# Performance work log

Hardware: AMD Instinct MI355X
Metric: run time of the kernel (lower is better)

Reference implementation:

```python
import jax, jax.numpy as jnp
import numpy as np

N, P, D_IN, K, D_H = 4, 20000, 1024, 8, 64


def setup_inputs() -> dict:
    key = jax.random.key(0)
    ks = jax.random.split(key, 10)
    inp = {
        "x": jax.random.normal(ks[0], (N, P, D_IN), dtype=jnp.float32),
        "centroids": jax.random.normal(ks[1], (K, D_IN), dtype=jnp.float32),
        # proj_pre: Linear(in_dim, 64) + ReLU  (W stored as [in, out])
        "W_pre": jax.random.normal(ks[2], (D_IN, D_H), dtype=jnp.float32) / np.sqrt(D_IN),
        "b_pre": jnp.zeros((D_H,), dtype=jnp.float32),
        # attention: Linear(64,32) -> Tanh -> Linear(32,1)
        "W_a1": jax.random.normal(ks[3], (D_H, 32), dtype=jnp.float32) / np.sqrt(D_H),
        "b_a1": jnp.zeros((32,), dtype=jnp.float32),
        "W_a2": jax.random.normal(ks[4], (32, 1), dtype=jnp.float32) / np.sqrt(32.0),
        "b_a2": jnp.zeros((1,), dtype=jnp.float32),
        # proj_out: Linear(64,32) + ReLU (+ Dropout, identity at eval)
        "W_out": jax.random.normal(ks[5], (D_H, 32), dtype=jnp.float32) / np.sqrt(D_H),
        "b_out": jnp.zeros((32,), dtype=jnp.float32),
    }
    return inp


def reference(x, centroids, W_pre, b_pre, W_a1, b_a1, W_a2, b_a2, W_out, b_out):
    # --- cdist-based hard cluster assignment ---------------------------------
    # ||x - c||: use the expanded form to avoid an [n,p,K,d] broadcast.
    x2 = jnp.sum(x * x, axis=-1)                       # [n, p]
    c2 = jnp.sum(centroids * centroids, axis=-1)       # [K]
    d2 = x2[..., None] + c2 - 2.0 * jnp.einsum('npd,kd->npk', x, centroids)
    dist = jnp.sqrt(jnp.maximum(d2, 0.0))              # [n, p, K]

    wc = jax.nn.softmax(1e7 / dist, axis=-1)           # softmax(1e7/dist)
    wc = (wc > 0.5).astype(x.dtype)                    # hard assignment
    # F.normalize(p=1, dim=1): divide by per-(n,K) patch count (eps=1e-12)
    wc = wc / jnp.maximum(jnp.sum(wc, axis=1, keepdims=True), 1e-12)
    mask = jnp.sum(wc, axis=1) == 0                    # [n, K] empty clusters

    # --- per-patch projection -------------------------------------------------
    xp = jax.nn.relu(x @ W_pre + b_pre)                # [n, p, 64]

    # --- cluster pooling + attention ------------------------------------------
    x_cls = jnp.einsum('npd,nph->nhd', xp, wc)         # [n, K, 64]
    A = (jnp.tanh(x_cls @ W_a1 + b_a1) @ W_a2 + b_a2)[..., 0]  # [n, K]
    A = jnp.where(mask, jnp.asarray(-100000.0, A.dtype), A)
    wa = jax.nn.softmax(A, axis=-1)                    # [n, K]
    pooled = jnp.einsum('nhd,nh->nd', x_cls, wa)       # [n, 64]

    enc_cls = jax.nn.relu(pooled @ W_out + b_out)      # [n, 32] (dropout = eval)
    enc_seq = xp.reshape(-1, xp.shape[-1])             # [(n*p), 64]
    return enc_cls, enc_seq, enc_seq
```

## Files before the change

kernel.cpp:

```cpp
#include <hip/hip_runtime.h>
#include <math.h>

#define N_  4
#define P_  20000
#define DIN 1024
#define K_  8
#define DH  64
#define BP  128
#define NT  5

typedef float  f32x4 __attribute__((ext_vector_type(4)));
typedef short  s16x8 __attribute__((ext_vector_type(8)));
typedef unsigned int u32x4 __attribute__((ext_vector_type(4)));
typedef unsigned short ushort_t;


union FragU { u32x4 u; s16x8 s; };

__global__ __launch_bounds__(512) void k_pre(const float* __restrict__ W_pre,
                                             const float* __restrict__ centroids,
                                             float* __restrict__ ws) {
  const int t = threadIdx.x;
  const int b = blockIdx.x;
  if (b < 80) {
    const int c = b;
    ushort_t* Bth = (ushort_t*)(ws + 4096);
    ushort_t* Btl = (ushort_t*)(ws + 45056);
    for (int d = t; d < DIN; d += 512) {
      float v = 0.f;
      if (c < 64)      v = W_pre[(size_t)d * DH + c];
      else if (c < 72) v = centroids[(size_t)(c - 64) * DIN + d];
      unsigned u = __float_as_uint(v);
      unsigned r = u + 0x7FFFu + ((u >> 16) & 1u);
      unsigned hb = r & 0xFFFF0000u;
      float lo = v - __uint_as_float(hb);
      unsigned ul = __float_as_uint(lo);
      unsigned rl = ul + 0x7FFFu + ((ul >> 16) & 1u);
      Bth[(size_t)c * DIN + d] = (ushort_t)(hb >> 16);
      Btl[(size_t)c * DIN + d] = (ushort_t)(rl >> 16);
    }
  } else {
    int* gcnt = (int*)(ws + 2048);
    for (int i = t; i < N_ * K_ * DH; i += 512) ws[i] = 0.f;
    if (t < N_ * K_) gcnt[t] = 0;
    const int w = t >> 6, lane = t & 63;
    float s = 0.f;
    for (int d = lane; d < DIN; d += 64) {
      float v = centroids[(size_t)w * DIN + d];
      s += v * v;
    }
    for (int off = 32; off > 0; off >>= 1) s += __shfl_down(s, off, 64);
    if (lane == 0) ws[2080 + w] = s;
  }
}

__device__ __forceinline__ void cvt_split(const f32x4 a0, const f32x4 a1,
                                          FragU& ah, FragU& al) {
  float f[8];
#pragma unroll
  for (int e = 0; e < 4; ++e) { f[e] = a0[e]; f[4 + e] = a1[e]; }
#pragma unroll
  for (int q = 0; q < 4; ++q) {
    const unsigned u0 = __float_as_uint(f[2 * q]);
    const unsigned u1 = __float_as_uint(f[2 * q + 1]);
    ah.u[q] = (u0 >> 16) | (u1 & 0xFFFF0000u);
    const float l0 = f[2 * q]     - __uint_as_float(u0 & 0xFFFF0000u);
    const float l1 = f[2 * q + 1] - __uint_as_float(u1 & 0xFFFF0000u);
    al.u[q] = (__float_as_uint(l0) >> 16) | (__float_as_uint(l1) & 0xFFFF0000u);
  }
}

__global__ __launch_bounds__(256, 3) void k_main(
    const float* __restrict__ x, const float* __restrict__ b_pre,
    float* __restrict__ out1, float* __restrict__ out2, float* __restrict__ ws) {
  __shared__ float xp[BP * 65];
  __shared__ float sc[BP * 9];
  __shared__ int   assign_s[BP];
  __shared__ int   cnt8[K_];

  const int t = threadIdx.x;
  const int w = t >> 6, l = t & 63;
  const int m = l & 15, q4 = l >> 4;
  const int n = blockIdx.y;
  const int p0 = blockIdx.x * BP;
  const int validP = (P_ - p0) < BP ? (P_ - p0) : BP;

  const ushort_t* Bth = (const ushort_t*)(ws + 4096);
  const ushort_t* Btl = (const ushort_t*)(ws + 45056);

  if (t < K_) cnt8[t] = 0;

  f32x4 acc[2][NT];
#pragma unroll
  for (int rg = 0; rg < 2; ++rg)
#pragma unroll
    for (int tl = 0; tl < NT; ++tl) acc[rg][tl] = (f32x4){0.f, 0.f, 0.f, 0.f};

  const int r0 = p0 + 32 * w + m;
  const int r1 = r0 + 16;
  const int g0 = r0 < P_ ? r0 : P_ - 1;
  const int g1 = r1 < P_ ? r1 : P_ - 1;
  const float* xbase = x + (size_t)n * P_ * DIN + q4 * 8;
  const float* ap0 = xbase + (size_t)g0 * DIN;
  const float* ap1 = xbase + (size_t)g1 * DIN;

  const ushort_t* bhp[NT];
  const ushort_t* blp[NT];
#pragma unroll
  for (int tl = 0; tl < NT; ++tl) {
    const size_t off = (size_t)(tl * 16 + m) * DIN + q4 * 8;
    bhp[tl] = Bth + off;
    blp[tl] = Btl + off;
  }

#pragma unroll 4
  for (int ks = 0; ks < 32; ++ks) {
    const int ko = ks * 32;
    const f32x4 a00 = *(const f32x4*)(ap0 + ko);
    const f32x4 a01 = *(const f32x4*)(ap0 + ko + 4);
    const f32x4 a10 = *(const f32x4*)(ap1 + ko);
    const f32x4 a11 = *(const f32x4*)(ap1 + ko + 4);
    FragU bh[NT], bl[NT];
#pragma unroll
    for (int tl = 0; tl < NT; ++tl) {
      bh[tl].u = *(const u32x4*)(bhp[tl] + ko);
      bl[tl].u = *(const u32x4*)(blp[tl] + ko);
    }
    FragU ah0, al0, ah1, al1;
    cvt_split(a00, a01, ah0, al0);
    cvt_split(a10, a11, ah1, al1);
#pragma unroll
    for (int tl = 0; tl < NT; ++tl) {
      acc[0][tl] = __builtin_amdgcn_mfma_f32_16x16x32_bf16(ah0.s, bh[tl].s, acc[0][tl], 0, 0, 0);
      acc[1][tl] = __builtin_amdgcn_mfma_f32_16x16x32_bf16(ah1.s, bh[tl].s, acc[1][tl], 0, 0, 0);
    }
#pragma unroll
    for (int tl = 0; tl < NT; ++tl) {
      acc[0][tl] = __builtin_amdgcn_mfma_f32_16x16x32_bf16(ah0.s, bl[tl].s, acc[0][tl], 0, 0, 0);
      acc[1][tl] = __builtin_amdgcn_mfma_f32_16x16x32_bf16(ah1.s, bl[tl].s, acc[1][tl], 0, 0, 0);
    }
#pragma unroll
    for (int tl = 0; tl < NT; ++tl) {
      acc[0][tl] = __builtin_amdgcn_mfma_f32_16x16x32_bf16(al0.s, bh[tl].s, acc[0][tl], 0, 0, 0);
      acc[1][tl] = __builtin_amdgcn_mfma_f32_16x16x32_bf16(al1.s, bh[tl].s, acc[1][tl], 0, 0, 0);
    }
  }

#pragma unroll
  for (int tl = 0; tl < 4; ++tl) {
    const int col = tl * 16 + m;
    const float bb = b_pre[col];
#pragma unroll
    for (int rg = 0; rg < 2; ++rg) {
#pragma unroll
      for (int r = 0; r < 4; ++r) {
        const int row = 32 * w + 16 * rg + (q4 << 2) + r;
        float v = acc[rg][tl][r] + bb;
        v = v > 0.f ? v : 0.f;
        xp[row * 65 + col] = v;
        if (row < validP) {
          const size_t o = (((size_t)(n * P_ + p0 + row)) << 6) + col;
          out1[o] = v;
          out2[o] = v;
        }
      }
    }
  }
  if (m < K_) {
    const float cc = ws[2080 + m];
#pragma unroll
    for (int rg = 0; rg < 2; ++rg)
#pragma unroll
      for (int r = 0; r < 4; ++r) {
        const int row = 32 * w + 16 * rg + (q4 << 2) + r;
        sc[row * 9 + m] = cc - 2.f * acc[rg][4][r];
      }
  }
  __syncthreads();

  if (t < BP) {
    int a = -1;
    if (t < validP) {
      float best = 3.4e38f; int bk = 0;
#pragma unroll
      for (int k = 0; k < K_; ++k) {
        const float v = sc[t * 9 + k];
        if (v < best) { best = v; bk = k; }
      }
      a = bk;
      atomicAdd(&cnt8[bk], 1);
    }
    assign_s[t] = a;
  }
  __syncthreads();

  for (int task = t; task < K_ * DH; task += 256) {
    const int k = task >> 6, j = task & 63;
    float s = 0.f;
    for (int p = 0; p < BP; ++p)
      s += (assign_s[p] == k) ? xp[p * 65 + j] : 0.f;
    if (s != 0.f) atomicAdd(&ws[(n * K_ + k) * DH + j], s);
  }
  if (t < K_ && cnt8[t] > 0) atomicAdd((int*)(ws + 2048) + n * K_ + t, cnt8[t]);
}

__global__ __launch_bounds__(256) void k_final(
    const float* __restrict__ W_a1, const float* __restrict__ b_a1,
    const float* __restrict__ W_a2, const float* __restrict__ b_a2,
    const float* __restrict__ W_out, const float* __restrict__ b_out,
    const float* __restrict__ ws, float* __restrict__ enc_cls) {
  __shared__ float xc[N_ * K_ * DH];
  __shared__ float zs[N_ * K_ * 32];
  __shared__ float wa[N_ * K_];
  __shared__ float As[N_ * K_];
  __shared__ int   cnts[N_ * K_];
  __shared__ float pooled[N_ * DH];
  const int t = threadIdx.x;
  const float* gsum = ws;
  const int* gcnt = (const int*)(ws + 2048);

  if (t < N_ * K_) cnts[t] = gcnt[t];
  __syncthreads();
  for (int i = t; i < N_ * K_ * DH; i += 256) {
    const int nk = i >> 6;
    const int c = cnts[nk];
    xc[i] = (c > 0) ? gsum[i] / (float)c : 0.f;
  }
  __syncthreads();
  for (int i = t; i < N_ * K_ * 32; i += 256) {
    const int nk = i >> 5, h = i & 31;
    float z = b_a1[h];
    for (int j = 0; j < DH; ++j) z += xc[nk * DH + j] * W_a1[j * 32 + h];
    zs[i] = tanhf(z) * W_a2[h];
  }
  __syncthreads();
  if (t < N_ * K_) {
    float a = b_a2[0];
    for (int h = 0; h < 32; ++h) a += zs[t * 32 + h];
    As[t] = (cnts[t] > 0) ? a : -100000.f;
  }
  __syncthreads();
  if (t < N_) {
    float mx = -3.4e38f;
    for (int k = 0; k < K_; ++k) mx = fmaxf(mx, As[t * K_ + k]);
    float ssum = 0.f;
    float e[K_];
    for (int k = 0; k < K_; ++k) { e[k] = expf(As[t * K_ + k] - mx); ssum += e[k]; }
    for (int k = 0; k < K_; ++k) wa[t * K_ + k] = e[k] / ssum;
  }
  __syncthreads();
  {
    const int n = t >> 6, j = t & 63;
    float s = 0.f;
    for (int k = 0; k < K_; ++k) s += xc[(n * K_ + k) * DH + j] * wa[n * K_ + k];
    pooled[t] = s;
  }
  __syncthreads();
  if (t < N_ * 32) {
    const int n = t >> 5, o = t & 31;
    float s = b_out[o];
    for (int j = 0; j < DH; ++j) s += pooled[n * DH + j] * W_out[j * 32 + o];
    enc_cls[n * 32 + o] = fmaxf(s, 0.f);
  }
}

extern "C" void kernel_launch(void* const* d_in, const int* in_sizes, int n_in,
                              void* d_out, int out_size, void* d_ws, size_t ws_size,
                              hipStream_t stream) {
  const float* x         = (const float*)d_in[0];
  const float* centroids = (const float*)d_in[1];
  const float* W_pre     = (const float*)d_in[2];
  const float* b_pre     = (const float*)d_in[3];
  const float* W_a1      = (const float*)d_in[4];
  const float* b_a1      = (const float*)d_in[5];
  const float* W_a2      = (const float*)d_in[6];
  const float* b_a2      = (const float*)d_in[7];
  const float* W_out     = (const float*)d_in[8];
  const float* b_out     = (const float*)d_in[9];

  float* out     = (float*)d_out;
  float* ws      = (float*)d_ws;
  float* enc_cls = out;
  float* out1    = out + N_ * 32;
  float* out2    = out + N_ * 32 + (size_t)N_ * P_ * DH;

  hipLaunchKernelGGL(k_pre, dim3(81), dim3(512), 0, stream, W_pre, centroids, ws);
  hipLaunchKernelGGL(k_main, dim3((P_ + BP - 1) / BP, N_), dim3(256), 0, stream,
                     x, b_pre, out1, out2, ws);
  hipLaunchKernelGGL(k_final, dim3(1), dim3(256), 0, stream,
                     W_a1, b_a1, W_a2, b_a2, W_out, b_out, ws, enc_cls);
}
```

Before: 554.3 us.

## Software-pipeline the MFMA k-loop with register double-buffered prefetch

Restructures the main GEMM k-loop into a two-stage software pipeline. The bf16 hi/lo weight fragments for the next step and the x fragments two steps ahead are loaded into alternating register buffers while the current step's MFMAs run. A sched_barrier separates the issued loads from the MFMA block. Launch bounds are relaxed from 3 to 2 waves per SIMD so the extra registers fit, trading occupancy for in-wave latency hiding.

```diff
diff --git a/kernel.cpp b/kernel.cpp
--- a/kernel.cpp
+++ b/kernel.cpp
@@ -70,7 +70,49 @@
   }
 }
 
-__global__ __launch_bounds__(256, 3) void k_main(
+template<bool PFB, bool PFX>
+__device__ __forceinline__ void kstep(
+    int kob, int kox,
+    FragU* bhC, FragU* blC, FragU* bhN, FragU* blN,
+    f32x4& X0, f32x4& X1, f32x4& X2, f32x4& X3,
+    const float* __restrict__ ap0, const float* __restrict__ ap1,
+    const ushort_t* const* bhp, const ushort_t* const* blp,
+    f32x4 acc[2][NT]) {
+  if (PFB) {
+#pragma unroll
+    for (int tl = 0; tl < NT; ++tl) {
+      bhN[tl].u = *(const u32x4*)(bhp[tl] + kob);
+      blN[tl].u = *(const u32x4*)(blp[tl] + kob);
+    }
+  }
+  FragU ah0, al0, ah1, al1;
+  cvt_split(X0, X1, ah0, al0);
+  cvt_split(X2, X3, ah1, al1);
+  if (PFX) {
+    X0 = *(const f32x4*)(ap0 + kox);
+    X1 = *(const f32x4*)(ap0 + kox + 4);
+    X2 = *(const f32x4*)(ap1 + kox);
+    X3 = *(const f32x4*)(ap1 + kox + 4);
+  }
+  __builtin_amdgcn_sched_barrier(0);
+#pragma unroll
+  for (int tl = 0; tl < NT; ++tl) {
+    acc[0][tl] = __builtin_amdgcn_mfma_f32_16x16x32_bf16(ah0.s, bhC[tl].s, acc[0][tl], 0, 0, 0);
+    acc[1][tl] = __builtin_amdgcn_mfma_f32_16x16x32_bf16(ah1.s, bhC[tl].s, acc[1][tl], 0, 0, 0);
+  }
+#pragma unroll
+  for (int tl = 0; tl < NT; ++tl) {
+    acc[0][tl] = __builtin_amdgcn_mfma_f32_16x16x32_bf16(ah0.s, blC[tl].s, acc[0][tl], 0, 0, 0);
+    acc[1][tl] = __builtin_amdgcn_mfma_f32_16x16x32_bf16(ah1.s, blC[tl].s, acc[1][tl], 0, 0, 0);
+  }
+#pragma unroll
+  for (int tl = 0; tl < NT; ++tl) {
+    acc[0][tl] = __builtin_amdgcn_mfma_f32_16x16x32_bf16(al0.s, bhC[tl].s, acc[0][tl], 0, 0, 0);
+    acc[1][tl] = __builtin_amdgcn_mfma_f32_16x16x32_bf16(al1.s, bhC[tl].s, acc[1][tl], 0, 0, 0);
+  }
+}
+
+__global__ __launch_bounds__(256, 2) void k_main(
     const float* __restrict__ x, const float* __restrict__ b_pre,
     float* __restrict__ out1, float* __restrict__ out2, float* __restrict__ ws) {
   __shared__ float xp[BP * 65];
@@ -113,38 +155,35 @@
     blp[tl] = Btl + off;
   }
 
-#pragma unroll 4
-  for (int ks = 0; ks < 32; ++ks) {
-    const int ko = ks * 32;
-    const f32x4 a00 = *(const f32x4*)(ap0 + ko);
-    const f32x4 a01 = *(const f32x4*)(ap0 + ko + 4);
-    const f32x4 a10 = *(const f32x4*)(ap1 + ko);
-    const f32x4 a11 = *(const f32x4*)(ap1 + ko + 4);
-    FragU bh[NT], bl[NT];
-#pragma unroll
-    for (int tl = 0; tl < NT; ++tl) {
-      bh[tl].u = *(const u32x4*)(bhp[tl] + ko);
-      bl[tl].u = *(const u32x4*)(blp[tl] + ko);
-    }
-    FragU ah0, al0, ah1, al1;
-    cvt_split(a00, a01, ah0, al0);
-    cvt_split(a10, a11, ah1, al1);
-#pragma unroll
-    for (int tl = 0; tl < NT; ++tl) {
-      acc[0][tl] = __builtin_amdgcn_mfma_f32_16x16x32_bf16(ah0.s, bh[tl].s, acc[0][tl], 0, 0, 0);
-      acc[1][tl] = __builtin_amdgcn_mfma_f32_16x16x32_bf16(ah1.s, bh[tl].s, acc[1][tl], 0, 0, 0);
-    }
-#pragma unroll
-    for (int tl = 0; tl < NT; ++tl) {
-      acc[0][tl] = __builtin_amdgcn_mfma_f32_16x16x32_bf16(ah0.s, bl[tl].s, acc[0][tl], 0, 0, 0);
-      acc[1][tl] = __builtin_amdgcn_mfma_f32_16x16x32_bf16(ah1.s, bl[tl].s, acc[1][tl], 0, 0, 0);
-    }
-#pragma unroll
-    for (int tl = 0; tl < NT; ++tl) {
-      acc[0][tl] = __builtin_amdgcn_mfma_f32_16x16x32_bf16(al0.s, bh[tl].s, acc[0][tl], 0, 0, 0);
-      acc[1][tl] = __builtin_amdgcn_mfma_f32_16x16x32_bf16(al1.s, bh[tl].s, acc[1][tl], 0, 0, 0);
-    }
-  }
+  FragU bhA[NT], blA[NT], bhB[NT], blB[NT];
+  f32x4 Xa0, Xa1, Xa2, Xa3, Xb0, Xb1, Xb2, Xb3;
+
+#pragma unroll
+  for (int tl = 0; tl < NT; ++tl) {
+    bhA[tl].u = *(const u32x4*)(bhp[tl]);
+    blA[tl].u = *(const u32x4*)(blp[tl]);
+  }
+  Xa0 = *(const f32x4*)(ap0);      Xa1 = *(const f32x4*)(ap0 + 4);
+  Xa2 = *(const f32x4*)(ap1);      Xa3 = *(const f32x4*)(ap1 + 4);
+  Xb0 = *(const f32x4*)(ap0 + 32); Xb1 = *(const f32x4*)(ap0 + 36);
+  Xb2 = *(const f32x4*)(ap1 + 32); Xb3 = *(const f32x4*)(ap1 + 36);
+
+  for (int ks = 0; ks < 28; ks += 2) {
+    kstep<true, true>((ks + 1) * 32, (ks + 2) * 32,
+                      bhA, blA, bhB, blB, Xa0, Xa1, Xa2, Xa3,
+                      ap0, ap1, bhp, blp, acc);
+    kstep<true, true>((ks + 2) * 32, (ks + 3) * 32,
+                      bhB, blB, bhA, blA, Xb0, Xb1, Xb2, Xb3,
+                      ap0, ap1, bhp, blp, acc);
+  }
+  kstep<true, true >(29 * 32, 30 * 32, bhA, blA, bhB, blB, Xa0, Xa1, Xa2, Xa3,
+                     ap0, ap1, bhp, blp, acc);
+  kstep<true, true >(30 * 32, 31 * 32, bhB, blB, bhA, blA, Xb0, Xb1, Xb2, Xb3,
+                     ap0, ap1, bhp, blp, acc);
+  kstep<true, false>(31 * 32, 0,       bhA, blA, bhB, blB, Xa0, Xa1, Xa2, Xa3,
+                     ap0, ap1, bhp, blp, acc);
+  kstep<false, false>(0, 0,            bhB, blB, bhA, blA, Xb0, Xb1, Xb2, Xb3,
+                     ap0, ap1, bhp, blp, acc);
 
 #pragma unroll
   for (int tl = 0; tl < 4; ++tl) {
```

Result: no change. 561.8 us (+1.4%).
